# Kernel optimization log

Measured on AMD Instinct MI355X. Metric: run time of the kernel, lower is better.

Reference implementation:

```python
import jax, jax.numpy as jnp
import numpy as np

N_NODES = 50000
N_EDGES = 1_600_000
Q_MULT = 8          # charges_irreps = 8x0e
NODE_MULT = 64      # node_feat_irreps = 64x0e + 64x1o
RBF = 8             # edge_feats_irreps num_irreps
HID = 64            # FullyConnectedNet hidden width
W_NUMEL = 2 * Q_MULT  # edge_tp weight_numel: two uvu paths (0e->0e, 0e x 1o->1o), u=8


def setup_inputs() -> dict:
    key = jax.random.key(0)
    k = jax.random.split(key, 14)
    f = lambda kk, sh: jax.random.normal(kk, sh, dtype=jnp.float32)
    return {
        "node_feats": f(k[0], (N_NODES, NODE_MULT * 4)),          # 64 scalars + 64 vectors(3)
        "charges_0": f(k[1], (N_NODES, Q_MULT)),                  # unused in forward
        "charges_induced": f(k[2], (N_NODES, Q_MULT)),
        "edge_feats": f(k[3], (N_EDGES, RBF)),
        "edge_attrs": f(k[4], (N_EDGES, 4)),                      # Y0 (1) + Y1 (3)
        "field_feats": f(k[5], (N_NODES, RBF)),                   # unused in forward
        "mlp_w1": f(k[6], (RBF, HID)),
        "mlp_w2": f(k[7], (HID, HID)),
        "mlp_w3": f(k[8], (HID, HID)),
        "mlp_w4": f(k[9], (HID, W_NUMEL)),
        "W0": f(k[10], (Q_MULT, NODE_MULT)),                      # node_tp path 0e x 0e -> 0e
        "W1": f(k[11], (Q_MULT, NODE_MULT)),                      # node_tp path 1o x 1o -> 0e
        "edge_index": jax.random.randint(k[12], (2, N_EDGES), 0, N_NODES, dtype=jnp.int32),
        "batch": jnp.zeros((N_NODES,), dtype=jnp.int32),
    }


def reference(node_feats, charges_0, charges_induced, edge_feats, edge_attrs,
              field_feats, mlp_w1, mlp_w2, mlp_w3, mlp_w4, W0, W1,
              edge_index, batch):
    sender, receiver = edge_index[0], edge_index[1]
    num_nodes = node_feats.shape[0]

    # e3nn FullyConnectedNet: variance-normalized linear layers + silu
    h = edge_feats
    for w in (mlp_w1, mlp_w2, mlp_w3):
        h = jax.nn.silu(h @ (w / np.sqrt(np.float32(w.shape[0]))))
    tp_w = h @ (mlp_w4 / np.sqrt(np.float32(mlp_w4.shape[0])))   # [E, 16]
    w0, w1 = tp_w[:, :Q_MULT], tp_w[:, Q_MULT:]                   # per-edge path weights

    # edge_tp (uvu, external weights): gather sender charges, weighted CG product
    q_s = charges_induced[sender]                                  # [E, 8]
    mid0 = (w0 * q_s) * edge_attrs[:, :1]                          # [E, 8]    0e
    mid1 = (w1 * q_s)[:, :, None] * edge_attrs[:, None, 1:4]       # [E, 8, 3] 1o

    # scatter-sum messages to receiver nodes
    sum0 = jax.ops.segment_sum(mid0, receiver, num_segments=num_nodes)
    sum1 = jax.ops.segment_sum(mid1.reshape(-1, Q_MULT * 3), receiver,
                               num_segments=num_nodes).reshape(-1, Q_MULT, 3)

    # node_tp: FullyConnectedTensorProduct(8x0e+8x1o, 64x0e+64x1o -> 1x0e)
    node0 = node_feats[:, :NODE_MULT]                              # [N, 64]
    node1 = node_feats[:, NODE_MULT:].reshape(-1, NODE_MULT, 3)    # [N, 64, 3]
    c = 1.0 / np.sqrt(np.float32(Q_MULT * NODE_MULT * 2))          # path normalization
    e0 = jnp.einsum('nu,nv,uv->n', sum0, node0, W0)
    e1 = jnp.einsum('nuk,nvk,uv->n', sum1, node1, W1) / np.sqrt(np.float32(3.0))  # w3j(1,1,0)
    return c * (e0 + e1)                                           # [N] per-node energy
```

## Files before the change

kernel.cpp:

```cpp
#include <hip/hip_runtime.h>
#include <hip/hip_bf16.h>

typedef short short8 __attribute__((ext_vector_type(8)));
typedef float f32x4 __attribute__((ext_vector_type(4)));

static __device__ __forceinline__ float bf2f(unsigned int b) { return __uint_as_float(b << 16); }
static __device__ __forceinline__ short fb2s(float x) {
    unsigned u = __float_as_uint(x);
    return (short)((u + 0x7FFFu + ((u >> 16) & 1u)) >> 16);
}
static __device__ __forceinline__ short fb2s_fast(float x) {
    return (short)((__float_as_uint(x) + 0x8000u) >> 16);
}
static __device__ __forceinline__ float silu(float x) {
    return x * __builtin_amdgcn_rcpf(1.0f + __expf(-x));
}
static __device__ __forceinline__ float load1(const void* p, long off, int isbf) {
    return isbf ? bf2f(((const unsigned short*)p)[off]) : ((const float*)p)[off];
}
static __device__ __forceinline__ void load4(const void* p, long off, int isbf, float* o) {
    if (isbf) {
        uint2 v = *(const uint2*)((const unsigned short*)p + off);
        o[0]=bf2f(v.x&0xffffu); o[1]=bf2f(v.x>>16);
        o[2]=bf2f(v.y&0xffffu); o[3]=bf2f(v.y>>16);
    } else {
        float4 v = *(const float4*)((const float*)p + off);
        o[0]=v.x; o[1]=v.y; o[2]=v.z; o[3]=v.w;
    }
}
static __device__ __forceinline__ int detect_bf16(const void* nf) {
    const unsigned int* w = (const unsigned int*)nf;
    int lane = threadIdx.x & 63;
    unsigned int e = (w[lane] >> 7) & 0xFFu;
    unsigned long long m = __ballot(e >= 118u && e <= 132u);
    return __popcll(m) >= 32 ? 1 : 0;
}

#define NB 32
__global__ __launch_bounds__(256) void k_node(
    const void* __restrict__ nf, const void* __restrict__ W0, const void* __restrict__ W1,
    const void* __restrict__ w1, const void* __restrict__ w2,
    const void* __restrict__ w3, const void* __restrict__ w4,
    short* __restrict__ Bws, float* __restrict__ NA, float* __restrict__ acc, int n_nodes) {
    __shared__ float Nd0[NB * 68];
    __shared__ float Nd1[3 * NB * 68];
    __shared__ float W0L[8 * 68];
    __shared__ float W1L[8 * 68];
    const int tid = threadIdx.x;
    const int isbf = detect_bf16(nf);
    const long n0 = (long)blockIdx.x * NB;

    if (blockIdx.x < 44) {
        int idx = blockIdx.x * 256 + tid;
        int j = idx & 7, lane = (idx >> 3) & 63, tile = idx >> 9;
        int n16 = lane & 15, kq = lane >> 4;
        float v;
        if (tile < 4) {
            int k = kq * 8 + j, n = tile * 16 + n16;
            v = (k < 8) ? load1(w1, k * 64 + n, isbf) : 0.0f;
        } else if (tile < 12) {
            int t = (tile - 4) >> 1, kt = (tile - 4) & 1;
            int k = kt * 32 + kq * 8 + j, n = t * 16 + n16;
            v = load1(w2, k * 64 + n, isbf) * 0.125f;
        } else if (tile < 20) {
            int t = (tile - 12) >> 1, kt = (tile - 12) & 1;
            int k = kt * 32 + kq * 8 + j, n = t * 16 + n16;
            v = load1(w3, k * 64 + n, isbf) * 0.125f;
        } else {
            int kt = tile - 20;
            int k = kt * 32 + kq * 8 + j, n = n16;
            v = load1(w4, k * 16 + n, isbf) * 0.125f;
        }
        Bws[idx] = fb2s(v);
    }
    if (tid < NB) {
        long n = n0 + tid;
        if (n < n_nodes) acc[n] = 0.0f;
    }
    if (n0 >= n_nodes) return;

    for (int i = tid; i < 512; i += 256) {
        W0L[(i >> 6) * 68 + (i & 63)] = load1(W0, i, isbf);
        W1L[(i >> 6) * 68 + (i & 63)] = load1(W1, i, isbf);
    }
    if (isbf) {
        for (int i = tid; i < NB * 32; i += 256) {
            int node = i >> 5, c8 = (i & 31) * 8;
            long ng = n0 + node; if (ng > n_nodes - 1) ng = n_nodes - 1;
            uint4 v = *(const uint4*)((const unsigned short*)nf + ng * 256 + c8);
            float f[8];
            f[0]=bf2f(v.x&0xffffu); f[1]=bf2f(v.x>>16);
            f[2]=bf2f(v.y&0xffffu); f[3]=bf2f(v.y>>16);
            f[4]=bf2f(v.z&0xffffu); f[5]=bf2f(v.z>>16);
            f[6]=bf2f(v.w&0xffffu); f[7]=bf2f(v.w>>16);
            #pragma unroll
            for (int t = 0; t < 8; t++) {
                int col = c8 + t;
                if (col < 64) Nd0[node * 68 + col] = f[t];
                else {
                    int cc = col - 64, vv = cc / 3, kk = cc - vv * 3;
                    Nd1[(kk * NB + node) * 68 + vv] = f[t];
                }
            }
        }
    } else {
        for (int i = tid; i < NB * 64; i += 256) {
            int node = i >> 6, c4 = (i & 63) * 4;
            long ng = n0 + node; if (ng > n_nodes - 1) ng = n_nodes - 1;
            float4 v = *(const float4*)((const float*)nf + ng * 256 + c4);
            float f[4] = {v.x, v.y, v.z, v.w};
            #pragma unroll
            for (int t = 0; t < 4; t++) {
                int col = c4 + t;
                if (col < 64) Nd0[node * 68 + col] = f[t];
                else {
                    int cc = col - 64, vv = cc / 3, kk = cc - vv * 3;
                    Nd1[(kk * NB + node) * 68 + vv] = f[t];
                }
            }
        }
    }
    __syncthreads();

    const int wv = tid >> 6, lane = tid & 63;
    const int u = lane & 7, ln = lane >> 3;
    float sum[4] = {0.0f, 0.0f, 0.0f, 0.0f};

    if (wv == 0) {
        const float* w = &W0L[u * 68];
        for (int v0 = 0; v0 < 64; v0 += 4) {
            float4 w4 = *(const float4*)(w + v0);
            #pragma unroll
            for (int j = 0; j < 4; j++) {
                float4 nd = *(const float4*)&Nd0[(ln + 8 * j) * 68 + v0];
                sum[j] += w4.x * nd.x + w4.y * nd.y + w4.z * nd.z + w4.w * nd.w;
            }
        }
        #pragma unroll
        for (int j = 0; j < 4; j++) {
            long node = n0 + ln + 8 * j;
            if (node < n_nodes) NA[node * 32 + u] = sum[j] * 0.03125f;
        }
    } else {
        const int kk = wv - 1;
        const float* w = &W1L[u * 68];
        const float* nd1 = &Nd1[kk * NB * 68];
        for (int v0 = 0; v0 < 64; v0 += 4) {
            float4 w4 = *(const float4*)(w + v0);
            #pragma unroll
            for (int j = 0; j < 4; j++) {
                float4 nd = *(const float4*)&nd1[(ln + 8 * j) * 68 + v0];
                sum[j] += w4.x * nd.x + w4.y * nd.y + w4.z * nd.z + w4.w * nd.w;
            }
        }
        #pragma unroll
        for (int j = 0; j < 4; j++) {
            long node = n0 + ln + 8 * j;
            if (node < n_nodes) NA[node * 32 + 8 + u * 3 + kk] = sum[j] * 0.018042195912175804f;
        }
    }
}

__global__ __launch_bounds__(256) void k_edges_mfma(
    const void* __restrict__ ef, const void* __restrict__ ea, const void* __restrict__ qc,
    const int* __restrict__ eidx, const void* __restrict__ nf,
    const short* __restrict__ Bws, const float* __restrict__ NA,
    float* __restrict__ acc, int n_edges) {
    __shared__ short W[11264];
    __shared__ short Hs[4 * 2304];
    const int tid = threadIdx.x, lane = tid & 63, wv = tid >> 6;
    const int n16 = lane & 15, kq = lane >> 4;
    const int isbf = detect_bf16(nf);

    {
        const uint4* src = (const uint4*)Bws;
        uint4* dst = (uint4*)W;
        for (int i = tid; i < 1408; i += 256) dst[i] = src[i];
    }
    __syncthreads();

    const long E0 = (long)blockIdx.x * 128 + wv * 32;
    short* Hw = Hs + wv * 2304;

    int woff[4];
    #pragma unroll
    for (int t = 0; t < 4; t++)
        woff[t] = (((t * 2 + (n16 >> 3)) ^ (kq >> 1)) << 3) + (n16 & 7);
    const int rbit = (n16 >> 3) & 1;

    short8 a1[2];
    #pragma unroll
    for (int mt = 0; mt < 2; mt++) {
        short8 a = {0,0,0,0,0,0,0,0};
        if (kq == 0) {
            long e = E0 + mt * 16 + n16;
            if (e > n_edges - 1) e = n_edges - 1;
            if (isbf) {
                a = *(const short8*)((const unsigned short*)ef + e * 8);
            } else {
                const float* pe = (const float*)ef + e * 8;
                float4 v0 = *(const float4*)pe, v1 = *(const float4*)(pe + 4);
                a[0]=fb2s(v0.x); a[1]=fb2s(v0.y); a[2]=fb2s(v0.z); a[3]=fb2s(v0.w);
                a[4]=fb2s(v1.x); a[5]=fb2s(v1.y); a[6]=fb2s(v1.z); a[7]=fb2s(v1.w);
            }
        }
        a1[mt] = a;
    }

    const f32x4 zero = {0.0f, 0.0f, 0.0f, 0.0f};

    {
        f32x4 c1[2][4];
        #pragma unroll
        for (int t = 0; t < 4; t++) {
            short8 b = *(const short8*)(W + t * 512 + lane * 8);
            #pragma unroll
            for (int mt = 0; mt < 2; mt++)
                c1[mt][t] = __builtin_amdgcn_mfma_f32_16x16x32_bf16(a1[mt], b, zero, 0, 0, 0);
        }
        #pragma unroll
        for (int mt = 0; mt < 2; mt++)
            #pragma unroll
            for (int t = 0; t < 4; t++)
                #pragma unroll
                for (int r = 0; r < 4; r++) {
                    float v = silu(c1[mt][t][r] * 0.35355339059327373f);
                    Hw[(mt * 16 + kq * 4 + r) * 72 + woff[t]] = fb2s_fast(v);
                }
    }

    #pragma unroll
    for (int L = 0; L < 2; L++) {
        const int base = (L == 0) ? 4 : 12;
        short8 a[2][2];
        #pragma unroll
        for (int mt = 0; mt < 2; mt++)
            #pragma unroll
            for (int kt = 0; kt < 2; kt++)
                a[mt][kt] = *(const short8*)(Hw + (mt * 16 + n16) * 72 + (((kt * 4 + kq) ^ rbit) << 3));
        f32x4 c2[2][4];
        #pragma unroll
        for (int mt = 0; mt < 2; mt++)
            #pragma unroll
            for (int t = 0; t < 4; t++) c2[mt][t] = zero;
        #pragma unroll
        for (int kt = 0; kt < 2; kt++)
            #pragma unroll
            for (int t = 0; t < 4; t++) {
                short8 b = *(const short8*)(W + (base + t * 2 + kt) * 512 + lane * 8);
                #pragma unroll
                for (int mt = 0; mt < 2; mt++)
                    c2[mt][t] = __builtin_amdgcn_mfma_f32_16x16x32_bf16(a[mt][kt], b, c2[mt][t], 0, 0, 0);
            }
        #pragma unroll
        for (int mt = 0; mt < 2; mt++)
            #pragma unroll
            for (int t = 0; t < 4; t++)
                #pragma unroll
                for (int r = 0; r < 4; r++) {
                    float v = silu(c2[mt][t][r]);
                    Hw[(mt * 16 + kq * 4 + r) * 72 + woff[t]] = fb2s_fast(v);
                }
    }

    float* TP = (float*)Hw;
    {
        short8 a[2][2];
        #pragma unroll
        for (int mt = 0; mt < 2; mt++)
            #pragma unroll
            for (int kt = 0; kt < 2; kt++)
                a[mt][kt] = *(const short8*)(Hw + (mt * 16 + n16) * 72 + (((kt * 4 + kq) ^ rbit) << 3));
        f32x4 c4[2] = {zero, zero};
        #pragma unroll
        for (int kt = 0; kt < 2; kt++) {
            short8 b = *(const short8*)(W + (20 + kt) * 512 + lane * 8);
            #pragma unroll
            for (int mt = 0; mt < 2; mt++)
                c4[mt] = __builtin_amdgcn_mfma_f32_16x16x32_bf16(a[mt][kt], b, c4[mt], 0, 0, 0);
        }
        #pragma unroll
        for (int mt = 0; mt < 2; mt++)
            #pragma unroll
            for (int r = 0; r < 4; r++)
                TP[(mt * 16 + kq * 4 + r) * 20 + n16] = c4[mt][r];
    }

    {
        const int el = lane >> 1, h = lane & 1;
        const long e = E0 + el;
        long ec = e;
        if (ec > n_edges - 1) ec = n_edges - 1;
        const int s = eidx[ec];
        const int r = eidx[(long)n_edges + ec];

        float4 t0 = *(const float4*)(TP + el * 20 + h * 4);
        float4 t1 = *(const float4*)(TP + el * 20 + 8 + h * 4);
        float tp0[4] = {t0.x, t0.y, t0.z, t0.w};
        float tp1[4] = {t1.x, t1.y, t1.z, t1.w};

        float q[4];
        load4(qc, (long)s * 8 + h * 4, isbf, q);
        float eav[4];
        load4(ea, ec * 4, isbf, eav);

        const float* nr = NA + (long)r * 32;
        float4 n0 = *(const float4*)(nr + h * 4);
        float t12[12];
        *(float4*)(t12 + 0) = *(const float4*)(nr + 8 + h * 12);
        *(float4*)(t12 + 4) = *(const float4*)(nr + 12 + h * 12);
        *(float4*)(t12 + 8) = *(const float4*)(nr + 16 + h * 12);

        float n0a[4] = {n0.x, n0.y, n0.z, n0.w};
        float p = 0.0f;
        #pragma unroll
        for (int i = 0; i < 4; i++) {
            float d = eav[1] * t12[i * 3] + eav[2] * t12[i * 3 + 1] + eav[3] * t12[i * 3 + 2];
            p += tp0[i] * q[i] * eav[0] * n0a[i] + tp1[i] * q[i] * d;
        }
        p += __shfl_xor(p, 1);
        if (h == 0 && e < n_edges) atomicAdd(&acc[r], p);
    }
}

__global__ void k_out(const float* __restrict__ acc, void* __restrict__ out,
                      const void* __restrict__ nf, int n) {
    const int isbf = detect_bf16(nf);
    int i = blockIdx.x * 256 + threadIdx.x;
    if (i >= n) return;
    if (isbf) ((__hip_bfloat16*)out)[i] = __float2bfloat16(acc[i]);
    else      ((float*)out)[i] = acc[i];
}

extern "C" void kernel_launch(void* const* d_in, const int* in_sizes, int n_in,
                              void* d_out, int out_size, void* d_ws, size_t ws_size,
                              hipStream_t stream) {
    const void* node_feats      = d_in[0];
    const void* charges_induced = d_in[2];
    const void* edge_feats      = d_in[3];
    const void* edge_attrs      = d_in[4];
    const void* mlp_w1          = d_in[6];
    const void* mlp_w2          = d_in[7];
    const void* mlp_w3          = d_in[8];
    const void* mlp_w4          = d_in[9];
    const void* W0              = d_in[10];
    const void* W1              = d_in[11];
    const int*  edge_index      = (const int*)d_in[12];

    const int n_nodes = in_sizes[0] / 256;
    const int n_edges = in_sizes[3] / 8;

    short* Bws = (short*)d_ws;
    float* NA  = (float*)((char*)d_ws + 22528);
    float* acc = NA + (size_t)n_nodes * 32;

    int nblk = (n_nodes + NB - 1) / NB;
    if (nblk < 44) nblk = 44;
    k_node<<<nblk, 256, 0, stream>>>(node_feats, W0, W1,
        mlp_w1, mlp_w2, mlp_w3, mlp_w4, Bws, NA, acc, n_nodes);
    k_edges_mfma<<<(n_edges + 127) / 128, 256, 0, stream>>>(
        edge_feats, edge_attrs, charges_induced, edge_index, node_feats, Bws, NA, acc, n_edges);
    k_out<<<(n_nodes + 255) / 256, 256, 0, stream>>>(acc, d_out, node_feats, n_nodes);
}
```

Baseline: 339.0 us.

## Process two edge tiles per block, prefetch gathers early, transpose MFMA operands

The edge kernel now handles 256 edges per block in two passes, so the weight copy into shared memory is amortised over twice as many edges. Index, edge-attribute and node-gather loads are issued before the MLP matmuls, letting their latency overlap with compute. MFMA operands are swapped so each lane gets contiguous outputs, which allows packed bf16 conversion (v_cvt_pk_bf16_f32) and vectorised shared-memory stores. The first-layer scale is folded into the weights, and launch bounds request 4 blocks per CU. Halving the block count may reduce parallelism, and the extra registers held across the MLP may pressure occupancy.

```diff
diff --git a/kernel.cpp b/kernel.cpp
--- a/kernel.cpp
+++ b/kernel.cpp
@@ -9,8 +9,10 @@
     unsigned u = __float_as_uint(x);
     return (short)((u + 0x7FFFu + ((u >> 16) & 1u)) >> 16);
 }
-static __device__ __forceinline__ short fb2s_fast(float x) {
-    return (short)((__float_as_uint(x) + 0x8000u) >> 16);
+static __device__ __forceinline__ unsigned int pack2(float lo, float hi) {
+    unsigned int r;
+    asm("v_cvt_pk_bf16_f32 %0, %1, %2" : "=v"(r) : "v"(lo), "v"(hi));
+    return r;
 }
 static __device__ __forceinline__ float silu(float x) {
     return x * __builtin_amdgcn_rcpf(1.0f + __expf(-x));
@@ -57,7 +59,7 @@
         float v;
         if (tile < 4) {
             int k = kq * 8 + j, n = tile * 16 + n16;
-            v = (k < 8) ? load1(w1, k * 64 + n, isbf) : 0.0f;
+            v = (k < 8) ? load1(w1, k * 64 + n, isbf) * 0.35355339059327373f : 0.0f;
         } else if (tile < 12) {
             int t = (tile - 4) >> 1, kt = (tile - 4) & 1;
             int k = kt * 32 + kq * 8 + j, n = t * 16 + n16;
@@ -161,13 +163,13 @@
     }
 }
 
-__global__ __launch_bounds__(256) void k_edges_mfma(
+__global__ __launch_bounds__(256, 4) void k_edges_mfma(
     const void* __restrict__ ef, const void* __restrict__ ea, const void* __restrict__ qc,
     const int* __restrict__ eidx, const void* __restrict__ nf,
     const short* __restrict__ Bws, const float* __restrict__ NA,
     float* __restrict__ acc, int n_edges) {
-    __shared__ short W[11264];
-    __shared__ short Hs[4 * 2304];
+    __shared__ __align__(16) short W[11264];
+    __shared__ __align__(16) short Hs[4 * 2304];
     const int tid = threadIdx.x, lane = tid & 63, wv = tid >> 6;
     const int n16 = lane & 15, kq = lane >> 4;
     const int isbf = detect_bf16(nf);
@@ -179,147 +181,140 @@
     }
     __syncthreads();
 
-    const long E0 = (long)blockIdx.x * 128 + wv * 32;
     short* Hw = Hs + wv * 2304;
-
-    int woff[4];
-    #pragma unroll
-    for (int t = 0; t < 4; t++)
-        woff[t] = (((t * 2 + (n16 >> 3)) ^ (kq >> 1)) << 3) + (n16 & 7);
     const int rbit = (n16 >> 3) & 1;
-
-    short8 a1[2];
-    #pragma unroll
-    for (int mt = 0; mt < 2; mt++) {
-        short8 a = {0,0,0,0,0,0,0,0};
-        if (kq == 0) {
-            long e = E0 + mt * 16 + n16;
-            if (e > n_edges - 1) e = n_edges - 1;
-            if (isbf) {
-                a = *(const short8*)((const unsigned short*)ef + e * 8);
-            } else {
-                const float* pe = (const float*)ef + e * 8;
-                float4 v0 = *(const float4*)pe, v1 = *(const float4*)(pe + 4);
-                a[0]=fb2s(v0.x); a[1]=fb2s(v0.y); a[2]=fb2s(v0.z); a[3]=fb2s(v0.w);
-                a[4]=fb2s(v1.x); a[5]=fb2s(v1.y); a[6]=fb2s(v1.z); a[7]=fb2s(v1.w);
-            }
-        }
-        a1[mt] = a;
-    }
-
+    const int wrow = n16 * 72 + ((kq & 1) << 2);
     const f32x4 zero = {0.0f, 0.0f, 0.0f, 0.0f};
 
-    {
-        f32x4 c1[2][4];
-        #pragma unroll
-        for (int t = 0; t < 4; t++) {
-            short8 b = *(const short8*)(W + t * 512 + lane * 8);
-            #pragma unroll
-            for (int mt = 0; mt < 2; mt++)
-                c1[mt][t] = __builtin_amdgcn_mfma_f32_16x16x32_bf16(a1[mt], b, zero, 0, 0, 0);
-        }
-        #pragma unroll
-        for (int mt = 0; mt < 2; mt++)
-            #pragma unroll
-            for (int t = 0; t < 4; t++)
-                #pragma unroll
-                for (int r = 0; r < 4; r++) {
-                    float v = silu(c1[mt][t][r] * 0.35355339059327373f);
-                    Hw[(mt * 16 + kq * 4 + r) * 72 + woff[t]] = fb2s_fast(v);
-                }
-    }
-
-    #pragma unroll
-    for (int L = 0; L < 2; L++) {
-        const int base = (L == 0) ? 4 : 12;
-        short8 a[2][2];
-        #pragma unroll
-        for (int mt = 0; mt < 2; mt++)
-            #pragma unroll
-            for (int kt = 0; kt < 2; kt++)
-                a[mt][kt] = *(const short8*)(Hw + (mt * 16 + n16) * 72 + (((kt * 4 + kq) ^ rbit) << 3));
-        f32x4 c2[2][4];
-        #pragma unroll
-        for (int mt = 0; mt < 2; mt++)
-            #pragma unroll
-            for (int t = 0; t < 4; t++) c2[mt][t] = zero;
-        #pragma unroll
-        for (int kt = 0; kt < 2; kt++)
-            #pragma unroll
-            for (int t = 0; t < 4; t++) {
-                short8 b = *(const short8*)(W + (base + t * 2 + kt) * 512 + lane * 8);
-                #pragma unroll
-                for (int mt = 0; mt < 2; mt++)
-                    c2[mt][t] = __builtin_amdgcn_mfma_f32_16x16x32_bf16(a[mt][kt], b, c2[mt][t], 0, 0, 0);
-            }
-        #pragma unroll
-        for (int mt = 0; mt < 2; mt++)
-            #pragma unroll
-            for (int t = 0; t < 4; t++)
-                #pragma unroll
-                for (int r = 0; r < 4; r++) {
-                    float v = silu(c2[mt][t][r]);
-                    Hw[(mt * 16 + kq * 4 + r) * 72 + woff[t]] = fb2s_fast(v);
-                }
-    }
-
-    float* TP = (float*)Hw;
-    {
-        short8 a[2][2];
-        #pragma unroll
-        for (int mt = 0; mt < 2; mt++)
-            #pragma unroll
-            for (int kt = 0; kt < 2; kt++)
-                a[mt][kt] = *(const short8*)(Hw + (mt * 16 + n16) * 72 + (((kt * 4 + kq) ^ rbit) << 3));
-        f32x4 c4[2] = {zero, zero};
-        #pragma unroll
-        for (int kt = 0; kt < 2; kt++) {
-            short8 b = *(const short8*)(W + (20 + kt) * 512 + lane * 8);
-            #pragma unroll
-            for (int mt = 0; mt < 2; mt++)
-                c4[mt] = __builtin_amdgcn_mfma_f32_16x16x32_bf16(a[mt][kt], b, c4[mt], 0, 0, 0);
-        }
-        #pragma unroll
-        for (int mt = 0; mt < 2; mt++)
-            #pragma unroll
-            for (int r = 0; r < 4; r++)
-                TP[(mt * 16 + kq * 4 + r) * 20 + n16] = c4[mt][r];
-    }
-
-    {
+    for (int half = 0; half < 2; half++) {
+        const long E0 = (long)blockIdx.x * 256 + half * 128 + wv * 32;
+
         const int el = lane >> 1, h = lane & 1;
-        const long e = E0 + el;
-        long ec = e;
-        if (ec > n_edges - 1) ec = n_edges - 1;
-        const int s = eidx[ec];
-        const int r = eidx[(long)n_edges + ec];
-
-        float4 t0 = *(const float4*)(TP + el * 20 + h * 4);
-        float4 t1 = *(const float4*)(TP + el * 20 + 8 + h * 4);
-        float tp0[4] = {t0.x, t0.y, t0.z, t0.w};
-        float tp1[4] = {t1.x, t1.y, t1.z, t1.w};
-
-        float q[4];
-        load4(qc, (long)s * 8 + h * 4, isbf, q);
+        const long e_ep = E0 + el;
+        long ec = e_ep; if (ec > n_edges - 1) ec = n_edges - 1;
+        const int s_nd = eidx[ec];
+        const int r_nd = eidx[(long)n_edges + ec];
         float eav[4];
         load4(ea, ec * 4, isbf, eav);
 
-        const float* nr = NA + (long)r * 32;
+        short8 a1[2];
+        #pragma unroll
+        for (int nt = 0; nt < 2; nt++) {
+            short8 a = {0,0,0,0,0,0,0,0};
+            if (kq == 0) {
+                long e = E0 + nt * 16 + n16;
+                if (e > n_edges - 1) e = n_edges - 1;
+                if (isbf) {
+                    a = *(const short8*)((const unsigned short*)ef + e * 8);
+                } else {
+                    const float* pe = (const float*)ef + e * 8;
+                    float4 v0 = *(const float4*)pe, v1 = *(const float4*)(pe + 4);
+                    a[0]=fb2s(v0.x); a[1]=fb2s(v0.y); a[2]=fb2s(v0.z); a[3]=fb2s(v0.w);
+                    a[4]=fb2s(v1.x); a[5]=fb2s(v1.y); a[6]=fb2s(v1.z); a[7]=fb2s(v1.w);
+                }
+            }
+            a1[nt] = a;
+        }
+
+        {
+            f32x4 c1[2][4];
+            #pragma unroll
+            for (int t = 0; t < 4; t++) {
+                short8 b = *(const short8*)(W + t * 512 + lane * 8);
+                #pragma unroll
+                for (int nt = 0; nt < 2; nt++)
+                    c1[nt][t] = __builtin_amdgcn_mfma_f32_16x16x32_bf16(b, a1[nt], zero, 0, 0, 0);
+            }
+            #pragma unroll
+            for (int nt = 0; nt < 2; nt++)
+                #pragma unroll
+                for (int t = 0; t < 4; t++) {
+                    uint2 pkd;
+                    pkd.x = pack2(silu(c1[nt][t][0]), silu(c1[nt][t][1]));
+                    pkd.y = pack2(silu(c1[nt][t][2]), silu(c1[nt][t][3]));
+                    *(uint2*)(Hw + nt * 1152 + wrow + (((t * 2 + (kq >> 1)) ^ rbit) << 3)) = pkd;
+                }
+        }
+
+        float q[4];
+        load4(qc, (long)s_nd * 8 + h * 4, isbf, q);
+        const float* nr = NA + (long)r_nd * 32;
         float4 n0 = *(const float4*)(nr + h * 4);
         float t12[12];
         *(float4*)(t12 + 0) = *(const float4*)(nr + 8 + h * 12);
         *(float4*)(t12 + 4) = *(const float4*)(nr + 12 + h * 12);
         *(float4*)(t12 + 8) = *(const float4*)(nr + 16 + h * 12);
 
-        float n0a[4] = {n0.x, n0.y, n0.z, n0.w};
-        float p = 0.0f;
         #pragma unroll
-        for (int i = 0; i < 4; i++) {
-            float d = eav[1] * t12[i * 3] + eav[2] * t12[i * 3 + 1] + eav[3] * t12[i * 3 + 2];
-            p += tp0[i] * q[i] * eav[0] * n0a[i] + tp1[i] * q[i] * d;
-        }
-        p += __shfl_xor(p, 1);
-        if (h == 0 && e < n_edges) atomicAdd(&acc[r], p);
+        for (int L = 0; L < 2; L++) {
+            const int base = (L == 0) ? 4 : 12;
+            short8 aH[2][2];
+            #pragma unroll
+            for (int nt = 0; nt < 2; nt++)
+                #pragma unroll
+                for (int kt = 0; kt < 2; kt++)
+                    aH[nt][kt] = *(const short8*)(Hw + nt * 1152 + n16 * 72 + (((kt * 4 + kq) ^ rbit) << 3));
+            f32x4 c2[2][4];
+            #pragma unroll
+            for (int nt = 0; nt < 2; nt++)
+                #pragma unroll
+                for (int t = 0; t < 4; t++) c2[nt][t] = zero;
+            #pragma unroll
+            for (int kt = 0; kt < 2; kt++)
+                #pragma unroll
+                for (int t = 0; t < 4; t++) {
+                    short8 b = *(const short8*)(W + (base + t * 2 + kt) * 512 + lane * 8);
+                    #pragma unroll
+                    for (int nt = 0; nt < 2; nt++)
+                        c2[nt][t] = __builtin_amdgcn_mfma_f32_16x16x32_bf16(b, aH[nt][kt], c2[nt][t], 0, 0, 0);
+                }
+            #pragma unroll
+            for (int nt = 0; nt < 2; nt++)
+                #pragma unroll
+                for (int t = 0; t < 4; t++) {
+                    uint2 pkd;
+                    pkd.x = pack2(silu(c2[nt][t][0]), silu(c2[nt][t][1]));
+                    pkd.y = pack2(silu(c2[nt][t][2]), silu(c2[nt][t][3]));
+                    *(uint2*)(Hw + nt * 1152 + wrow + (((t * 2 + (kq >> 1)) ^ rbit) << 3)) = pkd;
+                }
+        }
+
+        float* TP = (float*)Hw;
+        {
+            short8 aH[2][2];
+            #pragma unroll
+            for (int nt = 0; nt < 2; nt++)
+                #pragma unroll
+                for (int kt = 0; kt < 2; kt++)
+                    aH[nt][kt] = *(const short8*)(Hw + nt * 1152 + n16 * 72 + (((kt * 4 + kq) ^ rbit) << 3));
+            f32x4 c4[2] = {zero, zero};
+            #pragma unroll
+            for (int kt = 0; kt < 2; kt++) {
+                short8 b = *(const short8*)(W + (20 + kt) * 512 + lane * 8);
+                #pragma unroll
+                for (int nt = 0; nt < 2; nt++)
+                    c4[nt] = __builtin_amdgcn_mfma_f32_16x16x32_bf16(b, aH[nt][kt], c4[nt], 0, 0, 0);
+            }
+            #pragma unroll
+            for (int nt = 0; nt < 2; nt++)
+                *(f32x4*)(TP + (nt * 16 + n16) * 20 + (kq << 2)) = c4[nt];
+        }
+
+        {
+            float4 t0 = *(const float4*)(TP + el * 20 + h * 4);
+            float4 t1 = *(const float4*)(TP + el * 20 + 8 + h * 4);
+            float tp0[4] = {t0.x, t0.y, t0.z, t0.w};
+            float tp1[4] = {t1.x, t1.y, t1.z, t1.w};
+            float n0a[4] = {n0.x, n0.y, n0.z, n0.w};
+            float p = 0.0f;
+            #pragma unroll
+            for (int i = 0; i < 4; i++) {
+                float d = eav[1] * t12[i * 3] + eav[2] * t12[i * 3 + 1] + eav[3] * t12[i * 3 + 2];
+                p += tp0[i] * q[i] * eav[0] * n0a[i] + tp1[i] * q[i] * d;
+            }
+            p += __shfl_xor(p, 1);
+            if (h == 0 && e_ep < n_edges) atomicAdd(&acc[r_nd], p);
+        }
     }
 }
 
@@ -358,7 +353,7 @@
     if (nblk < 44) nblk = 44;
     k_node<<<nblk, 256, 0, stream>>>(node_feats, W0, W1,
         mlp_w1, mlp_w2, mlp_w3, mlp_w4, Bws, NA, acc, n_nodes);
-    k_edges_mfma<<<(n_edges + 127) / 128, 256, 0, stream>>>(
+    k_edges_mfma<<<(n_edges + 255) / 256, 256, 0, stream>>>(
         edge_feats, edge_attrs, charges_induced, edge_index, node_feats, Bws, NA, acc, n_edges);
     k_out<<<(n_nodes + 255) / 256, 256, 0, stream>>>(acc, d_out, node_feats, n_nodes);
 }
```

Measured after the change: 317.9 us. 6.2% less time.
